# Performance work log

Hardware: AMD Instinct MI355X
Metric: run time of the kernel (lower is better)

Reference implementation:

```python
import jax, jax.numpy as jnp
import numpy as np
from jax import lax

C = 256
HEADS = 8
HD = C // HEADS  # 32
D = 32  # max(L=32, C//16)
KERNELS = [1, 3, 5, 7]
EPS = 1e-5


def setup_inputs() -> dict:
    key = jax.random.key(0)
    ks = jax.random.split(key, 16)
    inp = {
        'x': jax.random.normal(ks[0], (8, C, 32, 32), jnp.float32),
        'qkv_w': jax.random.normal(ks[1], (3 * C, C), jnp.float32) * 0.05,
        'out_w': jax.random.normal(ks[2], (C, C), jnp.float32) * 0.05,
        'conv_w1': jax.random.normal(ks[3], (C, C, 1, 1), jnp.float32) * 0.05,
        'conv_w3': jax.random.normal(ks[4], (C, C, 3, 3), jnp.float32) * 0.05,
        'conv_w5': jax.random.normal(ks[5], (C, C, 5, 5), jnp.float32) * 0.05,
        'conv_w7': jax.random.normal(ks[6], (C, C, 7, 7), jnp.float32) * 0.05,
        'conv_b': jax.random.normal(ks[7], (4, C), jnp.float32) * 0.05,
        'bn_gamma': jax.random.uniform(ks[8], (4, C), jnp.float32, 0.5, 1.5),
        'bn_beta': jax.random.normal(ks[9], (4, C), jnp.float32) * 0.05,
        'bn_mean': jax.random.normal(ks[10], (4, C), jnp.float32) * 0.05,
        'bn_var': jax.random.uniform(ks[11], (4, C), jnp.float32, 0.5, 1.5),
        'fc_w': jax.random.normal(ks[12], (D, C), jnp.float32) * 0.05,
        'fc_b': jax.random.normal(ks[13], (D,), jnp.float32) * 0.05,
        'fcs_w': jax.random.normal(ks[14], (4, C, D), jnp.float32) * 0.05,
        'fcs_b': jax.random.normal(ks[15], (4, C), jnp.float32) * 0.05,
    }
    return inp


def _conv_bn_relu(x, w, b, g, beta, m, v):
    k = w.shape[-1]
    y = lax.conv_general_dilated(
        x, w, window_strides=(1, 1), padding=[(k // 2, k // 2)] * 2,
        dimension_numbers=('NCHW', 'OIHW', 'NCHW'))
    y = y + b[None, :, None, None]
    inv = g / jnp.sqrt(v + EPS)  # eval-mode batchnorm
    y = y * inv[None, :, None, None] + (beta - m * inv)[None, :, None, None]
    return jax.nn.relu(y)


def reference(x, qkv_w, out_w, conv_w1, conv_w3, conv_w5, conv_w7, conv_b,
              bn_gamma, bn_beta, bn_mean, bn_var, fc_w, fc_b, fcs_w, fcs_b):
    bsz, ch, ht, wd = x.shape
    n = ht * wd
    xf = x.reshape(bsz, ch, n)
    qkv = jnp.einsum('oc,bcn->bon', qkv_w, xf)  # [b, 3C, N] (1x1 conv)
    q, k, v = jnp.split(qkv, 3, axis=1)
    q = q.reshape(bsz, HEADS, HD, n)
    k = k.reshape(bsz, HEADS, HD, n)
    v = v.reshape(bsz, HEADS, HD, n)
    scale = 1.0 / np.sqrt(HD)
    scores = jnp.einsum('bhdi,bhdj->bhij', q, k) * scale  # [b,h,N,N]
    probs = jax.nn.softmax(scores, axis=-1)
    ctx = jnp.einsum('bhij,bhdj->bhdi', probs, v)  # [b,h,hd,N]
    ctx = ctx.reshape(bsz, ch, ht, wd)
    out = jnp.einsum('oc,bcn->bon', out_w, ctx.reshape(bsz, ch, n)).reshape(bsz, ch, ht, wd)

    ws = [conv_w1, conv_w3, conv_w5, conv_w7]
    feats = jnp.stack([
        _conv_bn_relu(out, ws[i], conv_b[i], bn_gamma[i], bn_beta[i], bn_mean[i], bn_var[i])
        for i in range(4)
    ], axis=0)  # [4, b, C, H, W]
    U = feats.sum(axis=0)
    S = U.mean(axis=(-2, -1))  # [b, C]
    Z = S @ fc_w.T + fc_b  # [b, D]
    logits = jnp.einsum('kcd,bd->kbc', fcs_w, Z) + fcs_b[:, None, :]  # [4,b,C]
    attn = jax.nn.softmax(logits, axis=0)[:, :, :, None, None]  # softmax over kernel branches
    V = (attn * feats).sum(axis=0)  # [b, C, H, W]
    return V
```

## Files before the change

### kernel.cpp

```cpp
#include <hip/hip_runtime.h>
#include <math.h>


typedef __attribute__((ext_vector_type(8))) short bf16x8;
typedef __attribute__((ext_vector_type(4))) float f32x4;

__device__ __forceinline__ ushort f2bf(float f) {
  uint32_t u = __float_as_uint(f);
  u += 0x7fffu + ((u >> 16) & 1u);
  return (ushort)(u >> 16);
}

__device__ __forceinline__ uint cvt_pk(float lo, float hi) {
  uint r;
  asm volatile("v_cvt_pk_bf16_f32 %0, %1, %2" : "=v"(r) : "v"(lo), "v"(hi));
  return r;
}


template <int KK>
__device__ __forceinline__ void repack_dev(const float* __restrict__ src,
                                           ushort* __restrict__ dst, int M, int co,
                                           char* smraw) {
  ushort(*t)[KK + 1] = (ushort(*)[KK + 1])smraw;
  int tid = threadIdx.x;
  for (int idx = tid; idx < 256 * KK; idx += 256) {
    int ci = idx / KK, k = idx - ci * KK;
    t[ci][k] = f2bf(src[(size_t)co * 256 * KK + idx]);
  }
  __syncthreads();
  for (int idx = tid; idx < 256 * KK; idx += 256) {
    int k = idx >> 8, ci = idx & 255;
    dst[((size_t)k * M + co) * 256 + ci] = t[ci][k];
  }
}

__device__ __forceinline__ void pad_dev(const float* __restrict__ src,
                                        ushort* __restrict__ dst, int y, int b,
                                        char* smraw) {
  ushort(*t)[258] = (ushort(*)[258])smraw;
  int tid = threadIdx.x;
  for (int u = 0; u < 32; ++u) {
    int idx = u * 256 + tid;
    int c = idx >> 5, p = idx & 31;
    t[p][c] = f2bf(src[(((size_t)b * 256 + c) << 10) + (y << 5) + p]);
  }
  __syncthreads();
  for (int u = 0; u < 32; ++u) {
    int idx = u * 256 + tid;
    int p = idx >> 8, c = idx & 255;
    dst[(((size_t)b * 38 + y + 3) * 38 + p + 3) * 256 + c] = t[p][c];
  }
}

__global__ __launch_bounds__(256) void prep_all(
    const float* __restrict__ qkv_w, const float* __restrict__ out_w,
    const float* __restrict__ cw1, const float* __restrict__ cw3,
    const float* __restrict__ cw5, const float* __restrict__ cw7,
    ushort* __restrict__ Wq, ushort* __restrict__ Wo, ushort* __restrict__ Wc,
    const float* __restrict__ x, ushort* __restrict__ P1,
    const float* __restrict__ cb, const float* __restrict__ g,
    const float* __restrict__ be, const float* __restrict__ mn,
    const float* __restrict__ v, float* __restrict__ binv, float* __restrict__ bb2) {
  __shared__ __align__(16) char sm[25600];
  int gx = blockIdx.x;
  if (gx < 768) repack_dev<1>(qkv_w, Wq, 768, gx, sm);
  else if (gx < 1024) repack_dev<1>(out_w, Wo, 256, gx - 768, sm);
  else if (gx < 1280) repack_dev<1>(cw1, Wc, 256, gx - 1024, sm);
  else if (gx < 1536) repack_dev<9>(cw3, Wc + 65536, 256, gx - 1280, sm);
  else if (gx < 1792) repack_dev<25>(cw5, Wc + 655360, 256, gx - 1536, sm);
  else if (gx < 2048) repack_dev<49>(cw7, Wc + 2293760, 256, gx - 1792, sm);
  else if (gx < 2304) pad_dev(x, P1, (gx - 2048) & 31, (gx - 2048) >> 5, sm);
  else if (gx == 2304) {
    int tid = threadIdx.x;
#pragma unroll
    for (int u = 0; u < 4; ++u) {
      int i = u * 256 + tid;
      float inv = g[i] * rsqrtf(v[i] + 1e-5f);
      binv[i] = inv;
      bb2[i] = be[i] + (cb[i] - mn[i]) * inv;
    }
  } else {
    int z = gx - 2305;
    int b = z >> 3;
    int part = z & 7;
    uint4* b4 = (uint4*)(P1 + (size_t)b * 369664);
    uint4 z4; z4.x = z4.y = z4.z = z4.w = 0u;
    for (int q = 0; q < 7; ++q) {
      int idx = q * 256 + threadIdx.x;
      if (idx < 1680) {
        int uidx = part * 1680 + idx;
        int p = uidx >> 5, ch = uidx & 31;
        int y, xx;
        if (p < 114) { y = p / 38; xx = p - y * 38; }
        else if (p < 306) {
          int r = p - 114; int ry = r / 6; int xi = r - ry * 6;
          y = 3 + ry; xx = xi < 3 ? xi : xi + 32;
        } else {
          int r = p - 306; int ry = r / 38; y = 35 + ry; xx = r - ry * 38;
        }
        b4[(y * 38 + xx) * 32 + ch] = z4;
      }
    }
  }
}

template <int MODE>
__device__ __forceinline__ void conv_core(
    const ushort* __restrict__ W, const ushort* __restrict__ X,
    float* __restrict__ outF, ushort* __restrict__ outU,
    int M, int KS, int b, int co0, int pxt, int cs0, int cs1, bool accum,
    char* smem) {
  const int R = KS >> 1;
  const int NT = KS * KS;
  const int NR = 4 + 2 * R;
  const int NPIX = NR * 38;
  char* Bs = smem;
  char* As = smem + 24320;
  const int tid = threadIdx.x;
  const int w = tid >> 6, l = tid & 63, lr = l & 15, sg = l >> 4;
  const int y0 = pxt * 4;
  const ushort* Xb = X + ((size_t)b * 38 + (y0 + 3 - R)) * 38 * 256;

  f32x4 acc[4][4] = {};

  auto stageA = [&](int t, int ci0, int bufsel) {
    const ushort* Wt = W + ((size_t)t * M + co0) * 256 + ci0;
    char* dbase = As + (bufsel << 13) + (w << 11);
#pragma unroll
    for (int u = 0; u < 2; ++u) {
      int idx16 = (w * 2 + u) * 64 + l;
      int co = idx16 >> 2, s = idx16 & 3;
      const ushort* src = Wt + (size_t)co * 256 + ((s ^ ((co >> 1) & 3)) << 3);
      __builtin_amdgcn_global_load_lds(
          (const __attribute__((address_space(1))) void*)src,
          (__attribute__((address_space(3))) void*)(dbase + (u << 10)), 16, 0, 0);
    }
  };

  int g = 0;
  stageA(0, cs0 << 5, 0);
  const int u_stg = (NPIX * 4 + 255) >> 8;
  for (int cs = cs0; cs < cs1; ++cs) {
    int ci0 = cs << 5;
    for (int u = 0; u < u_stg; ++u) {
      int idx = (u << 8) + tid;
      if (idx < NPIX * 4) {
        int pix = idx >> 2, s = idx & 3;
        int pr = pix / 38, pc = pix - pr * 38;
        const ushort* srcp = Xb + ((size_t)(pr * 38 + pc)) * 256 + ci0 +
                             ((s ^ ((pc >> 1) & 3)) << 3);
        __builtin_amdgcn_global_load_lds(
            (const __attribute__((address_space(1))) void*)srcp,
            (__attribute__((address_space(3))) void*)(Bs + (u << 12) + (w << 10)),
            16, 0, 0);
      }
    }
    __syncthreads();
    int dy = 0, dx = 0;
    for (int t = 0; t < NT; ++t) {
      bool staged = true;
      if (t + 1 < NT) stageA(t + 1, ci0, (g + 1) & 1);
      else if (cs + 1 < cs1) stageA(0, ci0 + 32, (g + 1) & 1);
      else staged = false;
      if (staged)
        asm volatile("s_waitcnt vmcnt(2)\n\ts_barrier" ::: "memory");
      else
        asm volatile("s_waitcnt vmcnt(0)\n\ts_barrier" ::: "memory");

      bf16x8 af[4], bfr[4];
      char* Ab = As + ((g & 1) << 13);
#pragma unroll
      for (int fa = 0; fa < 4; ++fa) {
        int co = (w & 1) * 64 + fa * 16 + lr;
        af[fa] = *(const bf16x8*)(Ab + (co << 6) + ((sg ^ ((co >> 1) & 3)) << 4));
      }
      int rowbase = (w >> 1) * 2 + dy;
      int cbase = dx + 3 - R + lr;
#pragma unroll
      for (int fp = 0; fp < 4; ++fp) {
        int lrow = rowbase + (fp >> 1);
        int pc = cbase + ((fp & 1) << 4);
        bfr[fp] = *(const bf16x8*)(Bs + ((lrow * 38 + pc) << 6) +
                                   ((sg ^ ((pc >> 1) & 3)) << 4));
      }
      __builtin_amdgcn_s_setprio(1);
#pragma unroll
      for (int fa = 0; fa < 4; ++fa)
#pragma unroll
        for (int fp = 0; fp < 4; ++fp)
          acc[fa][fp] = __builtin_amdgcn_mfma_f32_16x16x32_bf16(
              af[fa], bfr[fp], acc[fa][fp], 0, 0, 0);
      __builtin_amdgcn_s_setprio(0);
      ++g;
      if (++dx == KS) { dx = 0; ++dy; }
      asm volatile("s_barrier" ::: "memory");
    }
  }
  int coB = co0 + (w & 1) * 64;
  int pxB = pxt * 128 + (w >> 1) * 64;
#pragma unroll
  for (int fa = 0; fa < 4; ++fa) {
#pragma unroll
    for (int fp = 0; fp < 4; ++fp) {
      int px = pxB + (fp >> 1) * 32 + (fp & 1) * 16 + lr;
      int cobase = coB + fa * 16 + 4 * sg;
      f32x4 v4 = acc[fa][fp];
      if (MODE == 2) {
#pragma unroll
        for (int r = 0; r < 4; ++r) {
          int co = cobase + r;
          float* dst = &outF[((size_t)b * M + co) * 1024 + px];
          if (accum) unsafeAtomicAdd(dst, v4[r]);
          else *dst = v4[r];
        }
      } else if (MODE == 1) {
        int y = px >> 5, x = px & 31;
        ushort* dst = outU + ((size_t)(b * 38 + y + 3) * 38 + x + 3) * 256 + cobase;
        *(uint*)dst = cvt_pk(v4[0], v4[1]);
        *(uint*)(dst + 2) = cvt_pk(v4[2], v4[3]);
      } else {
        if (coB < 256) {
          int h = cobase >> 5, d = cobase & 31;
          ushort* dst = outU + ((size_t)(b * 8 + h) * 1024 + px) * 32 + d;
          const float sc = 0.17677669529663687f;
          *(uint*)dst = cvt_pk(v4[0] * sc, v4[1] * sc);
          *(uint*)(dst + 2) = cvt_pk(v4[2] * sc, v4[3] * sc);
        } else if (coB < 512) {
          int c2 = cobase - 256;
          int h = c2 >> 5, d = c2 & 31;
          ushort* dst = outU + 2097152 + ((size_t)(b * 8 + h) * 1024 + px) * 32 + d;
          *(uint*)dst = cvt_pk(v4[0], v4[1]);
          *(uint*)(dst + 2) = cvt_pk(v4[2], v4[3]);
        } else {
          int c2 = cobase - 512;
#pragma unroll
          for (int r = 0; r < 4; ++r)
            outU[4194304 + ((size_t)(b * 256 + c2 + r)) * 1024 + px] = f2bf(v4[r]);
        }
      }
    }
  }
}

__global__ __launch_bounds__(256, 2) void gemm_qkv(const ushort* __restrict__ W,
                                                   const ushort* __restrict__ X,
                                                   ushort* __restrict__ U) {
  __shared__ __align__(16) char smem[40704];
  int cot = blockIdx.x >> 3, pxt = blockIdx.x & 7, b = blockIdx.y;
  conv_core<0>(W, X, nullptr, U, 768, 1, b, cot * 128, pxt, 0, 8, false, smem);
}

__global__ __launch_bounds__(256, 2) void gemm_oproj(const ushort* __restrict__ W,
                                                     const ushort* __restrict__ X,
                                                     ushort* __restrict__ U) {
  __shared__ __align__(16) char smem[40704];
  int cot = blockIdx.x >> 3, pxt = blockIdx.x & 7, b = blockIdx.y;
  conv_core<1>(W, X, nullptr, U, 256, 1, b, cot * 128, pxt, 0, 8, false, smem);
}

__global__ __launch_bounds__(256, 4) void conv_fused(const ushort* __restrict__ Wc,
                                                     const ushort* __restrict__ X,
                                                     float* __restrict__ feats) {
  __shared__ __align__(16) char smem[40704];
  int gx = blockIdx.x;
  int sub = gx & 127;
  int pxt = sub & 7, cot = (sub >> 3) & 1, b = sub >> 4;
  int br, cs0, cs1;
  if (gx < 512) {
    br = 3; int ch = gx >> 7; cs0 = ch * 2; cs1 = cs0 + 2;
  } else if (gx < 768) {
    br = 2; int ch = (gx >> 7) & 1; cs0 = ch * 4; cs1 = cs0 + 4;
  } else {
    br = 1; int ch = (gx >> 7) & 1; cs0 = ch * 4; cs1 = cs0 + 4;
  }
  const int ksarr[4] = {1, 3, 5, 7};
  const int wofs[4] = {0, 65536, 655360, 2293760};
  conv_core<2>(Wc + wofs[br], X, feats + (size_t)br * 2097152, nullptr, 256,
               ksarr[br], b, cot * 128, pxt, cs0, cs1, true, smem);
  if (gx >= 768 && gx < 896) {
    __syncthreads();
    conv_core<2>(Wc, X, feats, nullptr, 256, 1, b, cot * 128, pxt, 0, 8, false,
                 smem);
  }
}

__global__ __launch_bounds__(256, 2) void flash_attn(const ushort* __restrict__ QKV,
                                                     ushort* __restrict__ P2out) {
  __shared__ __align__(16) char smem[24576];
  const int tid = threadIdx.x, w = tid >> 6, l = tid & 63, lr = l & 15, sg = l >> 4;
  char* Ks = smem;
  char* Vs = smem + 4096;
  char* Ps = smem + 8192 + (w << 12);
  int bh = blockIdx.y, b = bh >> 3, h = bh & 7;
  const ushort* QT = QKV + (size_t)bh * 32768;
  const ushort* KT = QKV + 2097152 + (size_t)bh * 32768;
  const ushort* VT = QKV + 4194304 + (size_t)(b * 256 + h * 32) * 1024;
  int ibase = blockIdx.x * 128 + w * 32;

  bf16x8 qf[2];
#pragma unroll
  for (int i16 = 0; i16 < 2; ++i16)
    qf[i16] = *(const bf16x8*)(QT + ((size_t)(ibase + i16 * 16 + lr)) * 32 + sg * 8);

  f32x4 oacc[4] = {};
  float mrow[2] = {-3e30f, -3e30f};
  float lrow[2] = {0.f, 0.f};

  for (int jb = 0; jb < 1024; jb += 64) {
    {
      int j = tid >> 2, s = tid & 3;
      const ushort* srcK = KT + (size_t)(jb + j) * 32 + ((s ^ ((j >> 1) & 3)) << 3);
      __builtin_amdgcn_global_load_lds(
          (const __attribute__((address_space(1))) void*)srcK,
          (__attribute__((address_space(3))) void*)(Ks + (w << 10)), 16, 0, 0);
      int d = tid >> 3, s2 = tid & 7;
      const ushort* srcV = VT + (size_t)d * 1024 + jb + ((s2 ^ (d & 7)) << 3);
      __builtin_amdgcn_global_load_lds(
          (const __attribute__((address_space(1))) void*)srcV,
          (__attribute__((address_space(3))) void*)(Vs + (w << 10)), 16, 0, 0);
    }
    __syncthreads();

    bf16x8 kf[4];
#pragma unroll
    for (int jt = 0; jt < 4; ++jt) {
      int j = jt * 16 + lr;
      kf[jt] = *(const bf16x8*)(Ks + j * 64 + ((sg ^ ((j >> 1) & 3)) << 4));
    }
    f32x4 sac[2][4] = {};
#pragma unroll
    for (int i16 = 0; i16 < 2; ++i16)
#pragma unroll
      for (int jt = 0; jt < 4; ++jt)
        sac[i16][jt] = __builtin_amdgcn_mfma_f32_16x16x32_bf16(
            kf[jt], qf[i16], sac[i16][jt], 0, 0, 0);

#pragma unroll
    for (int i16 = 0; i16 < 2; ++i16) {
      float tmax = sac[i16][0][0];
#pragma unroll
      for (int jt = 0; jt < 4; ++jt)
#pragma unroll
        for (int r = 0; r < 4; ++r) tmax = fmaxf(tmax, sac[i16][jt][r]);
      tmax = fmaxf(tmax, __shfl_xor(tmax, 16));
      tmax = fmaxf(tmax, __shfl_xor(tmax, 32));
      float mnew = fmaxf(mrow[i16], tmax);
      float fac = __expf(mrow[i16] - mnew);
      mrow[i16] = mnew;
      float psum = 0.f;
      int i = i16 * 16 + lr;
      char* prow = Ps + i * 128;
#pragma unroll
      for (int jt = 0; jt < 4; ++jt) {
        float p0 = __expf(sac[i16][jt][0] - mnew);
        float p1 = __expf(sac[i16][jt][1] - mnew);
        float p2 = __expf(sac[i16][jt][2] - mnew);
        float p3 = __expf(sac[i16][jt][3] - mnew);
        psum += (p0 + p1) + (p2 + p3);
        int j0 = jt * 16 + sg * 4;
        uint* dst = (uint*)(prow + (((j0 >> 3) ^ (i & 7)) << 4) + ((j0 & 7) << 1));
        dst[0] = cvt_pk(p0, p1);
        dst[1] = cvt_pk(p2, p3);
      }
      lrow[i16] = lrow[i16] * fac + psum;
#pragma unroll
      for (int d16 = 0; d16 < 2; ++d16)
#pragma unroll
        for (int r = 0; r < 4; ++r) oacc[d16 * 2 + i16][r] *= fac;
    }
    asm volatile("s_waitcnt lgkmcnt(0)" ::: "memory");

#pragma unroll
    for (int h2 = 0; h2 < 2; ++h2) {
      bf16x8 vf[2], pf[2];
#pragma unroll
      for (int d16 = 0; d16 < 2; ++d16) {
        int d = d16 * 16 + lr;
        vf[d16] = *(const bf16x8*)(Vs + d * 128 + ((((h2 << 2) + sg) ^ (d & 7)) << 4));
      }
#pragma unroll
      for (int i16 = 0; i16 < 2; ++i16) {
        int i = i16 * 16 + lr;
        pf[i16] = *(const bf16x8*)(Ps + i * 128 + ((((h2 << 2) + sg) ^ (i & 7)) << 4));
      }
#pragma unroll
      for (int d16 = 0; d16 < 2; ++d16)
#pragma unroll
        for (int i16 = 0; i16 < 2; ++i16)
          oacc[d16 * 2 + i16] = __builtin_amdgcn_mfma_f32_16x16x32_bf16(
              vf[d16], pf[i16], oacc[d16 * 2 + i16], 0, 0, 0);
    }
    __syncthreads();
  }

  float linv[2];
#pragma unroll
  for (int i16 = 0; i16 < 2; ++i16) {
    float lt = lrow[i16];
    lt += __shfl_xor(lt, 16);
    lt += __shfl_xor(lt, 32);
    linv[i16] = 1.0f / lt;
  }
#pragma unroll
  for (int i16 = 0; i16 < 2; ++i16) {
    int i = ibase + i16 * 16 + lr;
    int y = i >> 5, x = i & 31;
    ushort* dst0 = P2out + ((size_t)(b * 38 + y + 3) * 38 + x + 3) * 256 + h * 32 + sg * 4;
#pragma unroll
    for (int d16 = 0; d16 < 2; ++d16) {
      f32x4 v = oacc[d16 * 2 + i16];
      ushort* dst = dst0 + d16 * 16;
      *(uint*)dst = cvt_pk(v[0] * linv[i16], v[1] * linv[i16]);
      *(uint*)(dst + 2) = cvt_pk(v[2] * linv[i16], v[3] * linv[i16]);
    }
  }
}

__global__ __launch_bounds__(256) void reduce_s(const float* __restrict__ feats,
                                                const float* __restrict__ binv,
                                                const float* __restrict__ bb2,
                                                float* __restrict__ S) {
  int bc = blockIdx.x;
  int c = bc & 255;
  const float4* p4 = (const float4*)feats + (size_t)bc * 256;
  float s = 0;
#pragma unroll
  for (int k = 0; k < 4; ++k) {
    float bi = binv[k * 256 + c], bo = bb2[k * 256 + c];
    float4 v = p4[(size_t)k * 524288 + threadIdx.x];
    s += fmaxf(fmaf(v.x, bi, bo), 0.f) + fmaxf(fmaf(v.y, bi, bo), 0.f) +
         fmaxf(fmaf(v.z, bi, bo), 0.f) + fmaxf(fmaf(v.w, bi, bo), 0.f);
  }
  __shared__ float red[256];
  red[threadIdx.x] = s;
  __syncthreads();
  for (int off = 128; off > 0; off >>= 1) {
    if (threadIdx.x < off) red[threadIdx.x] += red[threadIdx.x + off];
    __syncthreads();
  }
  if (threadIdx.x == 0) S[bc] = red[0] * (1.0f / 1024.0f);
}

__global__ __launch_bounds__(256) void fc_attn_k(
    const float* __restrict__ S, const float* __restrict__ fc_w,
    const float* __restrict__ fc_b, const float* __restrict__ fcs_w,
    const float* __restrict__ fcs_b, float* __restrict__ attnw) {
  int b = blockIdx.x;
  __shared__ float Ss[256];
  __shared__ float Zs[32];
  int tid = threadIdx.x;
  Ss[tid] = S[b * 256 + tid];
  __syncthreads();
  if (tid < 32) {
    float z = fc_b[tid];
    for (int c = 0; c < 256; ++c) z += Ss[c] * fc_w[tid * 256 + c];
    Zs[tid] = z;
  }
  __syncthreads();
  int c = tid;
  float lg[4];
#pragma unroll
  for (int k = 0; k < 4; ++k) {
    float v = fcs_b[k * 256 + c];
    const float* wp = &fcs_w[((size_t)k * 256 + c) * 32];
#pragma unroll
    for (int d = 0; d < 32; ++d) v += wp[d] * Zs[d];
    lg[k] = v;
  }
  float m = fmaxf(fmaxf(lg[0], lg[1]), fmaxf(lg[2], lg[3]));
  float e0 = __expf(lg[0] - m), e1 = __expf(lg[1] - m);
  float e2 = __expf(lg[2] - m), e3 = __expf(lg[3] - m);
  float inv = 1.0f / (e0 + e1 + e2 + e3);
  attnw[(0 * 8 + b) * 256 + c] = e0 * inv;
  attnw[(1 * 8 + b) * 256 + c] = e1 * inv;
  attnw[(2 * 8 + b) * 256 + c] = e2 * inv;
  attnw[(3 * 8 + b) * 256 + c] = e3 * inv;
}

__global__ __launch_bounds__(256) void combine_k(const float* __restrict__ feats,
                                                 const float* __restrict__ attnw,
                                                 const float* __restrict__ binv,
                                                 const float* __restrict__ bb2,
                                                 float* __restrict__ out) {
  size_t i4 = (size_t)blockIdx.x * 256 + threadIdx.x;
  int c = (int)((i4 >> 8) & 255);
  int b = (int)(i4 >> 16);
  float4 s = {0.f, 0.f, 0.f, 0.f};
#pragma unroll
  for (int k = 0; k < 4; ++k) {
    float bi = binv[k * 256 + c], bo = bb2[k * 256 + c];
    float aw = attnw[(k * 8 + b) * 256 + c];
    float4 v = ((const float4*)feats)[(size_t)k * 524288 + i4];
    s.x += aw * fmaxf(fmaf(v.x, bi, bo), 0.f);
    s.y += aw * fmaxf(fmaf(v.y, bi, bo), 0.f);
    s.z += aw * fmaxf(fmaf(v.z, bi, bo), 0.f);
    s.w += aw * fmaxf(fmaf(v.w, bi, bo), 0.f);
  }
  ((float4*)out)[i4] = s;
}

extern "C" void kernel_launch(void* const* d_in, const int* in_sizes, int n_in,
                              void* d_out, int out_size, void* d_ws, size_t ws_size,
                              hipStream_t stream) {
  (void)in_sizes; (void)n_in; (void)out_size; (void)ws_size;
  const float* x      = (const float*)d_in[0];
  const float* qkv_w  = (const float*)d_in[1];
  const float* out_w  = (const float*)d_in[2];
  const float* cw1    = (const float*)d_in[3];
  const float* cw3    = (const float*)d_in[4];
  const float* cw5    = (const float*)d_in[5];
  const float* cw7    = (const float*)d_in[6];
  const float* conv_b = (const float*)d_in[7];
  const float* bn_g   = (const float*)d_in[8];
  const float* bn_b   = (const float*)d_in[9];
  const float* bn_m   = (const float*)d_in[10];
  const float* bn_v   = (const float*)d_in[11];
  const float* fc_w   = (const float*)d_in[12];
  const float* fc_b   = (const float*)d_in[13];
  const float* fcs_w  = (const float*)d_in[14];
  const float* fcs_b  = (const float*)d_in[15];

  char*  wsb   = (char*)d_ws;
  float* wsf   = (float*)d_ws;
  ushort* QKVb = (ushort*)d_ws;
  float* feats = wsf;
  float* S     = wsf + 10485760;
  float* attnw = wsf + 10487808;
  ushort* P1   = (ushort*)(wsb + 41984000);
  ushort* P2   = (ushort*)(wsb + 47898624);
  ushort* Wq   = (ushort*)(wsb + 53813248);
  ushort* Wo   = (ushort*)(wsb + 54206464);
  ushort* Wc   = (ushort*)(wsb + 54337536);
  float* binv  = (float*)(wsb + 65347584);
  float* bb2   = (float*)(wsb + 65351680);
  float* out   = (float*)d_out;

  prep_all<<<2369, 256, 0, stream>>>(qkv_w, out_w, cw1, cw3, cw5, cw7, Wq, Wo, Wc,
                                     x, P1, conv_b, bn_g, bn_b, bn_m, bn_v,
                                     binv, bb2);

  gemm_qkv<<<dim3(48, 8), 256, 0, stream>>>(Wq, P1, QKVb);
  flash_attn<<<dim3(8, 64), 256, 0, stream>>>(QKVb, P2);
  hipMemsetAsync(wsb + 8388608, 0, 25165824, stream);
  gemm_oproj<<<dim3(16, 8), 256, 0, stream>>>(Wo, P2, P1);
  conv_fused<<<dim3(1024), 256, 0, stream>>>(Wc, P1, feats);

  reduce_s<<<2048, 256, 0, stream>>>(feats, binv, bb2, S);
  fc_attn_k<<<8, 256, 0, stream>>>(S, fc_w, fc_b, fcs_w, fcs_b, attnw);
  combine_k<<<2048, 256, 0, stream>>>(feats, attnw, binv, bb2, out);
}
```

Measured before the change: 205.3 us.

## Stream K/V into registers with double buffering and fold memset into oproj

Flash attention now loads K and V fragments straight from global memory into registers, prefetching the next tile while computing the current one. This removes the LDS staging and the per-iteration barriers, and shrinks shared memory. Separately, the hipMemsetAsync that zeroes part of the workspace is dropped, and the gemm_oproj blocks zero that region themselves, saving a launch. The risks are more register pressure and K/V fetches that each wave issues redundantly instead of sharing them.

```diff
diff --git a/kernel.cpp b/kernel.cpp
--- a/kernel.cpp
+++ b/kernel.cpp
@@ -253,10 +253,16 @@
 
 __global__ __launch_bounds__(256, 2) void gemm_oproj(const ushort* __restrict__ W,
                                                      const ushort* __restrict__ X,
-                                                     ushort* __restrict__ U) {
+                                                     ushort* __restrict__ U,
+                                                     float* __restrict__ fz) {
   __shared__ __align__(16) char smem[40704];
   int cot = blockIdx.x >> 3, pxt = blockIdx.x & 7, b = blockIdx.y;
   conv_core<1>(W, X, nullptr, U, 256, 1, b, cot * 128, pxt, 0, 8, false, smem);
+  int blk = blockIdx.y * 16 + blockIdx.x;
+  float4* dst = (float4*)fz + (size_t)blk * 12288;
+  float4 z4 = {0.f, 0.f, 0.f, 0.f};
+#pragma unroll
+  for (int q = 0; q < 48; ++q) dst[q * 256 + threadIdx.x] = z4;
 }
 
 __global__ __launch_bounds__(256, 4) void conv_fused(const ushort* __restrict__ Wc,
@@ -287,11 +293,9 @@
 
 __global__ __launch_bounds__(256, 2) void flash_attn(const ushort* __restrict__ QKV,
                                                      ushort* __restrict__ P2out) {
-  __shared__ __align__(16) char smem[24576];
+  __shared__ __align__(16) char smem[16384];
   const int tid = threadIdx.x, w = tid >> 6, l = tid & 63, lr = l & 15, sg = l >> 4;
-  char* Ks = smem;
-  char* Vs = smem + 4096;
-  char* Ps = smem + 8192 + (w << 12);
+  char* Ps = smem + (w << 12);
   int bh = blockIdx.y, b = bh >> 3, h = bh & 7;
   const ushort* QT = QKV + (size_t)bh * 32768;
   const ushort* KT = QKV + 2097152 + (size_t)bh * 32768;
@@ -307,34 +311,33 @@
   float mrow[2] = {-3e30f, -3e30f};
   float lrow[2] = {0.f, 0.f};
 
-  for (int jb = 0; jb < 1024; jb += 64) {
-    {
-      int j = tid >> 2, s = tid & 3;
-      const ushort* srcK = KT + (size_t)(jb + j) * 32 + ((s ^ ((j >> 1) & 3)) << 3);
-      __builtin_amdgcn_global_load_lds(
-          (const __attribute__((address_space(1))) void*)srcK,
-          (__attribute__((address_space(3))) void*)(Ks + (w << 10)), 16, 0, 0);
-      int d = tid >> 3, s2 = tid & 7;
-      const ushort* srcV = VT + (size_t)d * 1024 + jb + ((s2 ^ (d & 7)) << 3);
-      __builtin_amdgcn_global_load_lds(
-          (const __attribute__((address_space(1))) void*)srcV,
-          (__attribute__((address_space(3))) void*)(Vs + (w << 10)), 16, 0, 0);
-    }
-    __syncthreads();
-
-    bf16x8 kf[4];
-#pragma unroll
-    for (int jt = 0; jt < 4; ++jt) {
-      int j = jt * 16 + lr;
-      kf[jt] = *(const bf16x8*)(Ks + j * 64 + ((sg ^ ((j >> 1) & 3)) << 4));
-    }
+  const ushort* Krow = KT + (size_t)lr * 32 + sg * 8;
+  const ushort* Vrow = VT + (size_t)lr * 1024 + sg * 8;
+
+  bf16x8 k0[4], v0[4], k1[4], v1[4];
+  auto LK = [&](int jb, bf16x8* kf) {
+#pragma unroll
+    for (int jt = 0; jt < 4; ++jt)
+      kf[jt] = *(const bf16x8*)(Krow + ((size_t)jb + jt * 16) * 32);
+  };
+  auto LV = [&](int jb, bf16x8* vf) {
+#pragma unroll
+    for (int d16 = 0; d16 < 2; ++d16)
+#pragma unroll
+      for (int h2 = 0; h2 < 2; ++h2)
+        vf[d16 * 2 + h2] =
+            *(const bf16x8*)(Vrow + (size_t)d16 * 16384 + jb + h2 * 32);
+  };
+
+  auto body = [&](int jb, bf16x8* kc, bf16x8* vc, bf16x8* kn, bf16x8* vn) {
+    if (jb + 64 < 1024) { LK(jb + 64, kn); LV(jb + 64, vn); }
     f32x4 sac[2][4] = {};
 #pragma unroll
     for (int i16 = 0; i16 < 2; ++i16)
 #pragma unroll
       for (int jt = 0; jt < 4; ++jt)
         sac[i16][jt] = __builtin_amdgcn_mfma_f32_16x16x32_bf16(
-            kf[jt], qf[i16], sac[i16][jt], 0, 0, 0);
+            kc[jt], qf[i16], sac[i16][jt], 0, 0, 0);
 
 #pragma unroll
     for (int i16 = 0; i16 < 2; ++i16) {
@@ -373,12 +376,7 @@
 
 #pragma unroll
     for (int h2 = 0; h2 < 2; ++h2) {
-      bf16x8 vf[2], pf[2];
-#pragma unroll
-      for (int d16 = 0; d16 < 2; ++d16) {
-        int d = d16 * 16 + lr;
-        vf[d16] = *(const bf16x8*)(Vs + d * 128 + ((((h2 << 2) + sg) ^ (d & 7)) << 4));
-      }
+      bf16x8 pf[2];
 #pragma unroll
       for (int i16 = 0; i16 < 2; ++i16) {
         int i = i16 * 16 + lr;
@@ -389,9 +387,16 @@
 #pragma unroll
         for (int i16 = 0; i16 < 2; ++i16)
           oacc[d16 * 2 + i16] = __builtin_amdgcn_mfma_f32_16x16x32_bf16(
-              vf[d16], pf[i16], oacc[d16 * 2 + i16], 0, 0, 0);
-    }
-    __syncthreads();
+              vc[d16 * 2 + h2], pf[i16], oacc[d16 * 2 + i16], 0, 0, 0);
+    }
+  };
+
+  LK(0, k0);
+  LV(0, v0);
+#pragma unroll 1
+  for (int jb = 0; jb < 1024; jb += 128) {
+    body(jb, k0, v0, k1, v1);
+    body(jb + 64, k1, v1, k0, v0);
   }
 
   float linv[2];
@@ -542,8 +547,7 @@
 
   gemm_qkv<<<dim3(48, 8), 256, 0, stream>>>(Wq, P1, QKVb);
   flash_attn<<<dim3(8, 64), 256, 0, stream>>>(QKVb, P2);
-  hipMemsetAsync(wsb + 8388608, 0, 25165824, stream);
-  gemm_oproj<<<dim3(16, 8), 256, 0, stream>>>(Wo, P2, P1);
+  gemm_oproj<<<dim3(16, 8), 256, 0, stream>>>(Wo, P2, P1, (float*)(wsb + 8388608));
   conv_fused<<<dim3(1024), 256, 0, stream>>>(Wc, P1, feats);
 
   reduce_s<<<2048, 256, 0, stream>>>(feats, binv, bb2, S);
```

Measured after the change: 200.9 us (median of 2 runs). -2.2%, faster.
